# Performance work log

Hardware: AMD Instinct MI355X
Metric: run time of the kernel (lower is better)

The kernel has to match this reference:

```python
import jax, jax.numpy as jnp
import numpy as np

VOCAB = 32000
DIM = 256
LAYERS = 2
CLASSES = 8
BATCH = 32
SEQ = 8192


def setup_inputs() -> dict:
    key = jax.random.key(0)
    ks = jax.random.split(key, 8)
    s = 1.0 / np.sqrt(DIM)
    x = jax.random.randint(ks[0], (BATCH, SEQ), 0, VOCAB, dtype=jnp.int32)
    emb = jax.random.normal(ks[1], (VOCAB, DIM), dtype=jnp.float32)
    Wz = jax.random.normal(ks[2], (LAYERS, DIM, DIM), dtype=jnp.float32) * s
    bz = jnp.zeros((LAYERS, DIM), dtype=jnp.float32)
    Wh = jax.random.normal(ks[3], (LAYERS, DIM, DIM), dtype=jnp.float32) * s
    bh = jnp.zeros((LAYERS, DIM), dtype=jnp.float32)
    Wo = jax.random.normal(ks[4], (DIM, CLASSES), dtype=jnp.float32) * s
    bo = jnp.zeros((CLASSES,), dtype=jnp.float32)
    return {"x": x, "emb": emb, "Wz": Wz, "bz": bz, "Wh": Wh, "bh": bh, "Wo": Wo, "bo": bo}


def _min_gru_layer(h_in, Wz_l, bz_l, Wh_l, bh_l):
    # minGRU: z_t = sigmoid(W_z x_t); h~_t = W_h x_t
    # h_t = (1 - z_t) * h_{t-1} + z_t * h~_t,  h_0 = 0
    z = jax.nn.sigmoid(jnp.einsum('bsd,de->bse', h_in, Wz_l) + bz_l)
    h_tilde = jnp.einsum('bsd,de->bse', h_in, Wh_l) + bh_l
    a = 1.0 - z          # decay coefficient
    b = z * h_tilde      # input contribution
    # parallel associative scan of h_t = a_t * h_{t-1} + b_t (h_0 = 0)
    def combine(c1, c2):
        a1, b1 = c1
        a2, b2 = c2
        return a1 * a2, b1 * a2 + b2
    _, h = jax.lax.associative_scan(combine, (a, b), axis=1)
    return h


def reference(x, emb, Wz, bz, Wh, bh, Wo, bo):
    h = emb[x]  # [B, S, D]
    for l in range(LAYERS):
        h = _min_gru_layer(h, Wz[l], bz[l], Wh[l], bh[l])
    # classifier on the last timestep
    return h[:, -1] @ Wo + bo  # [B, CLASSES]
```

## Files before the change

kernel.cpp:

```cpp
#include <hip/hip_runtime.h>
#include <stdint.h>

#define SEQ 8192
#define CS 64
#define NCH 128
#define NBLK 4096

typedef float f32x4 __attribute__((ext_vector_type(4)));
typedef short short8 __attribute__((ext_vector_type(8)));
typedef unsigned short u16;
typedef u16 ushort8 __attribute__((ext_vector_type(8)));
typedef u16 ushort4v __attribute__((ext_vector_type(4)));

__device__ __forceinline__ u16 f2bf(float f) {
  uint32_t u = __float_as_uint(f);
  u += 0x7fffu + ((u >> 16) & 1u);
  return (u16)(u >> 16);
}

__device__ __forceinline__ void gld16(void* lds, const void* g) {
  __builtin_amdgcn_global_load_lds(
      (const __attribute__((address_space(1))) uint32_t*)g,
      (__attribute__((address_space(3))) uint32_t*)lds, 16, 0, 0);
}

__global__ void embq_kernel(const float* __restrict__ emb, u16* __restrict__ embq) {
  int i = (blockIdx.x * 256 + threadIdx.x) * 4;
  float4 v = *(const float4*)(emb + i);
  ushort4v p;
  p[0] = f2bf(v.x); p[1] = f2bf(v.y); p[2] = f2bf(v.z); p[3] = f2bf(v.w);
  *(ushort4v*)(embq + i) = p;
}

__global__ void wt_kernel(const float* __restrict__ Wz, const float* __restrict__ Wh,
                          u16* __restrict__ WtS) {
  int idx = blockIdx.x * 256 + threadIdx.x;
  int d = idx & 255;
  int k = (idx >> 8) & 255;
  int m = idx >> 16;
  const float* src = (m < 2 ? Wz : Wh) + (size_t)(m & 1) * 65536;
  float v = src[k * 256 + d];
  int dh = d >> 6, dloc = d & 63, k32 = k >> 5, kl = k & 31;
  size_t tile = ((size_t)(m * 4 + dh) * 8 + k32) * 4096;
  size_t byte = (size_t)(dloc * 64 + ((kl * 2) ^ (((dloc >> 1) & 3) << 4)));
  *(u16*)((char*)WtS + tile + byte) = f2bf(v);
}

__device__ __forceinline__ void stage32(char* dst_wave, const char* WtSb, int mat, int k32,
                                        int w, int lane) {
  const char* src = WtSb + ((size_t)((mat * 4 + w) * 8 + k32)) * 4096 + lane * 16;
  #pragma unroll
  for (int i = 0; i < 4; i++)
    gld16(dst_wave + i * 1024, src + i * 1024);
}

__device__ __forceinline__ void load_fa(const u16* As, int k32, int l15, int lg,
                                        short8 (&fa)[4]) {
  const int xm = (l15 & 7) << 4;
  const int kt = k32 >> 1, ks = k32 & 1;
  #pragma unroll
  for (int mi = 0; mi < 4; mi++)
    fa[mi] = *(const short8*)((const char*)As + kt * 8192 +
               (((mi * 16 + l15) * 128 + ks * 64 + lg * 16) ^ xm));
}

__device__ __forceinline__ void mfma_frags(const char* Pw, const short8 (&fa)[4],
    int l15, int lg, f32x4 (&acc)[4][4])
{
  #pragma unroll
  for (int ni = 0; ni < 4; ni++) {
    const int dloc = ni * 16 + l15;
    const int off = dloc * 64 + ((lg * 16) ^ (((dloc >> 1) & 3) << 4));
    short8 fb = *(const short8*)(Pw + off);
    #pragma unroll
    for (int mi = 0; mi < 4; mi++)
      acc[mi][ni] = __builtin_amdgcn_mfma_f32_16x16x32_bf16(fa[mi], fb, acc[mi][ni], 0, 0, 0);
  }
}

__device__ __forceinline__ void gemm_pipe3(int lsel, const char* WtSb, const u16* As,
    char* Pw, int w, int l15, int lg, int lane,
    f32x4 (&accz)[4][4], f32x4 (&acch)[4][4])
{
  stage32(Pw,         WtSb, lsel,     0, w, lane);
  stage32(Pw + 16384, WtSb, 2 + lsel, 0, w, lane);
  short8 fa[4];
  #pragma unroll
  for (int i = 0; i < 16; ++i) {
    if (i < 15) asm volatile("s_waitcnt vmcnt(4)" ::: "memory");
    else        asm volatile("s_waitcnt vmcnt(0)" ::: "memory");
    __builtin_amdgcn_sched_barrier(0);
    if (i + 2 < 16)
      stage32(Pw + ((i + 2) % 3) * 16384, WtSb,
              ((i + 2) & 1) ? (2 + lsel) : lsel, (i + 2) >> 1, w, lane);
    if ((i & 1) == 0) {
      load_fa(As, i >> 1, l15, lg, fa);
      mfma_frags(Pw + (i % 3) * 16384, fa, l15, lg, accz);
    } else {
      mfma_frags(Pw + (i % 3) * 16384, fa, l15, lg, acch);
    }
  }
}

__device__ __forceinline__ float2* seg_ptr(char* segt, int s, int d) {
  return (float2*)(segt + s * 2048 + ((d * 8) ^ (s << 4)));
}

template<int PHASE>
__global__ __launch_bounds__(256, 2)
void gru_kernel(const int* __restrict__ x, const u16* __restrict__ embq,
                const u16* __restrict__ WtS,
                const float* __restrict__ bz0, const float* __restrict__ bh0,
                const float* __restrict__ bz1, const float* __restrict__ bh1,
                const float* __restrict__ carry,
                float* __restrict__ Ap, float* __restrict__ Bs)
{
  __shared__ __align__(16) u16 As[16384];
  __shared__ __align__(16) char Pb[49152];

  const int tid = threadIdx.x;
  const int lane = tid & 63;
  const int w = tid >> 6;
  const int l15 = lane & 15, lg = lane >> 4;
  const int cb = blockIdx.x;
  const int b = cb >> 7, c = cb & (NCH - 1);
  const char* WtSb = (const char*)WtS;
  char* segt = (char*)As;
  char* Pw = Pb + w * 4096;

  {
    const int sm = tid >> 2, kq = tid & 3;
    const int tok = x[b * SEQ + c * CS + sm];
    const u16* src = embq + (size_t)tok * 256 + kq * 64;
    char* sub = (char*)As + kq * 8192;
    const int swz = (sm & 7) << 4;
    #pragma unroll
    for (int j = 0; j < 8; j++) {
      ushort8 p = *(const ushort8*)(src + j * 8);
      *(ushort8*)(sub + ((sm * 128 + j * 16) ^ swz)) = p;
    }
  }

  f32x4 accz[4][4], acch[4][4];
  #pragma unroll
  for (int i = 0; i < 4; i++)
    #pragma unroll
    for (int j = 0; j < 4; j++) {
      f32x4 zz = {0.f, 0.f, 0.f, 0.f};
      accz[i][j] = zz; acch[i][j] = zz;
    }

  __syncthreads();
  gemm_pipe3(0, WtSb, As, Pw, w, l15, lg, lane, accz, acch);
  __syncthreads();

  #pragma unroll
  for (int ni = 0; ni < 4; ni++) {
    const int d = w * 64 + ni * 16 + l15;
    const float bzv = bz0[d];
    const float bhv = bh0[d];
    #pragma unroll
    for (int mi = 0; mi < 4; mi++) {
      float A = 1.f, B = 0.f;
      #pragma unroll
      for (int r = 0; r < 4; r++) {
        float zl = accz[mi][ni][r] + bzv;
        float a = __builtin_amdgcn_rcpf(1.f + __expf(zl));
        float ht = acch[mi][ni][r] + bhv;
        float bb = (1.f - a) * ht;
        if (PHASE == 1) { accz[mi][ni][r] = a; acch[mi][ni][r] = bb; }
        B = B * a + bb;
        A *= a;
      }
      *seg_ptr(segt, mi * 4 + lg, d) = make_float2(A, B);
    }
  }
  __syncthreads();

  if (PHASE == 0) {
    float PA = 1.f, PB = 0.f;
    #pragma unroll
    for (int s = 0; s < 16; s++) {
      float2 v = *seg_ptr(segt, s, tid);
      PB = v.x * PB + v.y;
      PA *= v.x;
    }
    Ap[(size_t)cb * 256 + tid] = PA;
    Bs[(size_t)cb * 256 + tid] = PB;
    return;
  }

  {
    float PA = 1.f, PB = 0.f;
    #pragma unroll
    for (int s = 0; s < 16; s++) {
      float2* p = seg_ptr(segt, s, tid);
      float2 v = *p;
      *p = make_float2(PA, PB);
      PB = v.x * PB + v.y;
      PA *= v.x;
    }
  }
  __syncthreads();

  float ea[4][4], eb[4][4], h0v[4];
  #pragma unroll
  for (int ni = 0; ni < 4; ni++) {
    const int d = w * 64 + ni * 16 + l15;
    h0v[ni] = carry[(size_t)cb * 256 + d];
    #pragma unroll
    for (int mi = 0; mi < 4; mi++) {
      float2 e = *seg_ptr(segt, mi * 4 + lg, d);
      ea[mi][ni] = e.x; eb[mi][ni] = e.y;
    }
  }
  __syncthreads();

  #pragma unroll
  for (int ni = 0; ni < 4; ni++) {
    const int d = w * 64 + ni * 16 + l15;
    char* sub = (char*)As + (d >> 6) * 8192;
    const int kl2 = (d & 63) * 2;
    #pragma unroll
    for (int mi = 0; mi < 4; mi++) {
      float h = ea[mi][ni] * h0v[ni] + eb[mi][ni];
      #pragma unroll
      for (int r = 0; r < 4; r++) {
        h = accz[mi][ni][r] * h + acch[mi][ni][r];
        const int t = mi * 16 + lg * 4 + r;
        *(u16*)(sub + ((t * 128 + kl2) ^ ((t & 7) << 4))) = f2bf(h);
      }
    }
  }

  #pragma unroll
  for (int i = 0; i < 4; i++)
    #pragma unroll
    for (int j = 0; j < 4; j++) {
      f32x4 zz = {0.f, 0.f, 0.f, 0.f};
      accz[i][j] = zz; acch[i][j] = zz;
    }

  __syncthreads();
  gemm_pipe3(1, WtSb, As, Pw, w, l15, lg, lane, accz, acch);
  __syncthreads();

  #pragma unroll
  for (int ni = 0; ni < 4; ni++) {
    const int d = w * 64 + ni * 16 + l15;
    const float bzv = bz1[d];
    const float bhv = bh1[d];
    #pragma unroll
    for (int mi = 0; mi < 4; mi++) {
      float A = 1.f, B = 0.f;
      #pragma unroll
      for (int r = 0; r < 4; r++) {
        float zl = accz[mi][ni][r] + bzv;
        float a = __builtin_amdgcn_rcpf(1.f + __expf(zl));
        float ht = acch[mi][ni][r] + bhv;
        float bb = (1.f - a) * ht;
        B = B * a + bb;
        A *= a;
      }
      *seg_ptr(segt, mi * 4 + lg, d) = make_float2(A, B);
    }
  }
  __syncthreads();
  {
    float PA = 1.f, PB = 0.f;
    #pragma unroll
    for (int s = 0; s < 16; s++) {
      float2 v = *seg_ptr(segt, s, tid);
      PB = v.x * PB + v.y;
      PA *= v.x;
    }
    Ap[(size_t)cb * 256 + tid] = PA;
    Bs[(size_t)cb * 256 + tid] = PB;
  }
}

__global__ void scan2_l0(const float* __restrict__ Ap0, const float* __restrict__ Bs0,
                         float* __restrict__ carry) {
  const int g = blockIdx.x * 256 + threadIdx.x;
  const int b = g >> 8, d = g & 255;
  float h = 0.f;
  for (int c = 0; c < NCH; c++) {
    const size_t idx = (size_t)(b * NCH + c) * 256 + d;
    carry[idx] = h;
    h = Bs0[idx] + Ap0[idx] * h;
  }
}

__global__ void scan2_l1(const float* __restrict__ Ap1, const float* __restrict__ Bs1,
                         float* __restrict__ hlast) {
  const int g = blockIdx.x * 256 + threadIdx.x;
  const int b = g >> 8, d = g & 255;
  float h = 0.f;
  for (int c = 0; c < NCH; c++) {
    const size_t idx = (size_t)(b * NCH + c) * 256 + d;
    h = Bs1[idx] + Ap1[idx] * h;
  }
  hlast[b * 256 + d] = h;
}

__global__ void cls_kernel(const float* __restrict__ hlast, const float* __restrict__ Wo,
                           const float* __restrict__ bo, float* __restrict__ out) {
  const int t = threadIdx.x;
  const int b = t >> 3, c = t & 7;
  float acc = bo[c];
  for (int d = 0; d < 256; d++) acc += hlast[b * 256 + d] * Wo[d * 8 + c];
  out[t] = acc;
}

extern "C" void kernel_launch(void* const* d_in, const int* in_sizes, int n_in,
                              void* d_out, int out_size, void* d_ws, size_t ws_size,
                              hipStream_t stream) {
  (void)in_sizes; (void)n_in; (void)out_size; (void)ws_size;
  const int*   x   = (const int*)d_in[0];
  const float* emb = (const float*)d_in[1];
  const float* Wz  = (const float*)d_in[2];
  const float* bz  = (const float*)d_in[3];
  const float* Wh  = (const float*)d_in[4];
  const float* bh  = (const float*)d_in[5];
  const float* Wo  = (const float*)d_in[6];
  const float* bo  = (const float*)d_in[7];
  float* out = (float*)d_out;
  char* ws = (char*)d_ws;

  u16*   embq  = (u16*)  (ws);
  u16*   WtS   = (u16*)  (ws + 16777216ull);
  float* Ap0   = (float*)(ws + 17301504ull);
  float* Bs0   = (float*)(ws + 21495808ull);
  float* carry = (float*)(ws + 25690112ull);
  float* Ap1   = (float*)(ws + 29884416ull);
  float* Bs1   = (float*)(ws + 34078720ull);
  float* hlast = (float*)(ws + 38273024ull);

  embq_kernel<<<8000, 256, 0, stream>>>(emb, embq);
  wt_kernel<<<1024, 256, 0, stream>>>(Wz, Wh, WtS);

  gru_kernel<0><<<NBLK, 256, 0, stream>>>(
      x, embq, WtS, bz, bh, bz + 256, bh + 256, nullptr, Ap0, Bs0);
  scan2_l0<<<32, 256, 0, stream>>>(Ap0, Bs0, carry);
  gru_kernel<1><<<NBLK, 256, 0, stream>>>(
      x, embq, WtS, bz, bh, bz + 256, bh + 256, carry, Ap1, Bs1);

  scan2_l1<<<32, 256, 0, stream>>>(Ap1, Bs1, hlast);
  cls_kernel<<<1, 256, 0, stream>>>(hlast, Wo, bo, out);
}
```

Baseline: 291.7 us.

## Stash layer-0 gate coefficients in global memory instead of recomputing the layer-0 GEMM

Phase 0 now writes per-timestep (a, b) coefficients as packed bf16 pairs into a workspace buffer. Phase 1 reads them back and runs a simple sequential per-channel recurrence instead of redoing the embedding gather and layer-0 GEMM. To keep that buffer small enough to stay cache-resident, the batch is processed in two halves with separate launches. The trade is extra global traffic, bf16 rounding of the coefficients, and twice as many kernel launches, in exchange for dropping the duplicate layer-0 GEMM.

```diff
diff --git a/kernel.cpp b/kernel.cpp
--- a/kernel.cpp
+++ b/kernel.cpp
@@ -4,7 +4,8 @@
 #define SEQ 8192
 #define CS 64
 #define NCH 128
-#define NBLK 4096
+#define HB2 16
+#define HBLK (HB2 * NCH)
 
 typedef float f32x4 __attribute__((ext_vector_type(4)));
 typedef short short8 __attribute__((ext_vector_type(8)));
@@ -16,6 +17,9 @@
   uint32_t u = __float_as_uint(f);
   u += 0x7fffu + ((u >> 16) & 1u);
   return (u16)(u >> 16);
+}
+__device__ __forceinline__ float bf2f(uint32_t lo16) {
+  return __uint_as_float(lo16 << 16);
 }
 
 __device__ __forceinline__ void gld16(void* lds, const void* g) {
@@ -112,7 +116,7 @@
                 const u16* __restrict__ WtS,
                 const float* __restrict__ bz0, const float* __restrict__ bh0,
                 const float* __restrict__ bz1, const float* __restrict__ bh1,
-                const float* __restrict__ carry,
+                const float* __restrict__ carry, uint32_t* __restrict__ ab,
                 float* __restrict__ Ap, float* __restrict__ Bs)
 {
   __shared__ __align__(16) u16 As[16384];
@@ -128,19 +132,6 @@
   char* segt = (char*)As;
   char* Pw = Pb + w * 4096;
 
-  {
-    const int sm = tid >> 2, kq = tid & 3;
-    const int tok = x[b * SEQ + c * CS + sm];
-    const u16* src = embq + (size_t)tok * 256 + kq * 64;
-    char* sub = (char*)As + kq * 8192;
-    const int swz = (sm & 7) << 4;
-    #pragma unroll
-    for (int j = 0; j < 8; j++) {
-      ushort8 p = *(const ushort8*)(src + j * 8);
-      *(ushort8*)(sub + ((sm * 128 + j * 16) ^ swz)) = p;
-    }
-  }
-
   f32x4 accz[4][4], acch[4][4];
   #pragma unroll
   for (int i = 0; i < 4; i++)
@@ -150,97 +141,74 @@
       accz[i][j] = zz; acch[i][j] = zz;
     }
 
-  __syncthreads();
-  gemm_pipe3(0, WtSb, As, Pw, w, l15, lg, lane, accz, acch);
-  __syncthreads();
-
-  #pragma unroll
-  for (int ni = 0; ni < 4; ni++) {
-    const int d = w * 64 + ni * 16 + l15;
-    const float bzv = bz0[d];
-    const float bhv = bh0[d];
-    #pragma unroll
-    for (int mi = 0; mi < 4; mi++) {
-      float A = 1.f, B = 0.f;
+  if (PHASE == 0) {
+    {
+      const int sm = tid >> 2, kq = tid & 3;
+      const int tok = x[b * SEQ + c * CS + sm];
+      const u16* src = embq + (size_t)tok * 256 + kq * 64;
+      char* sub = (char*)As + kq * 8192;
+      const int swz = (sm & 7) << 4;
       #pragma unroll
-      for (int r = 0; r < 4; r++) {
-        float zl = accz[mi][ni][r] + bzv;
-        float a = __builtin_amdgcn_rcpf(1.f + __expf(zl));
-        float ht = acch[mi][ni][r] + bhv;
-        float bb = (1.f - a) * ht;
-        if (PHASE == 1) { accz[mi][ni][r] = a; acch[mi][ni][r] = bb; }
-        B = B * a + bb;
-        A *= a;
+      for (int j = 0; j < 8; j++) {
+        ushort8 p = *(const ushort8*)(src + j * 8);
+        *(ushort8*)(sub + ((sm * 128 + j * 16) ^ swz)) = p;
       }
-      *seg_ptr(segt, mi * 4 + lg, d) = make_float2(A, B);
-    }
-  }
-  __syncthreads();
-
-  if (PHASE == 0) {
-    float PA = 1.f, PB = 0.f;
-    #pragma unroll
-    for (int s = 0; s < 16; s++) {
-      float2 v = *seg_ptr(segt, s, tid);
-      PB = v.x * PB + v.y;
-      PA *= v.x;
-    }
-    Ap[(size_t)cb * 256 + tid] = PA;
-    Bs[(size_t)cb * 256 + tid] = PB;
+    }
+    __syncthreads();
+    gemm_pipe3(0, WtSb, As, Pw, w, l15, lg, lane, accz, acch);
+    __syncthreads();
+
+    #pragma unroll
+    for (int ni = 0; ni < 4; ni++) {
+      const int d = w * 64 + ni * 16 + l15;
+      const float bzv = bz0[d];
+      const float bhv = bh0[d];
+      #pragma unroll
+      for (int mi = 0; mi < 4; mi++) {
+        float A = 1.f, B = 0.f;
+        #pragma unroll
+        for (int r = 0; r < 4; r++) {
+          float zl = accz[mi][ni][r] + bzv;
+          float a = __builtin_amdgcn_rcpf(1.f + __expf(zl));
+          float ht = acch[mi][ni][r] + bhv;
+          float bb = (1.f - a) * ht;
+          const int t = mi * 16 + lg * 4 + r;
+          ab[(size_t)cb * 16384 + t * 256 + d] =
+              (uint32_t)f2bf(a) | ((uint32_t)f2bf(bb) << 16);
+          B = B * a + bb;
+          A *= a;
+        }
+        *seg_ptr(segt, mi * 4 + lg, d) = make_float2(A, B);
+      }
+    }
+    __syncthreads();
+    {
+      float PA = 1.f, PB = 0.f;
+      #pragma unroll
+      for (int s = 0; s < 16; s++) {
+        float2 v = *seg_ptr(segt, s, tid);
+        PB = v.x * PB + v.y;
+        PA *= v.x;
+      }
+      Ap[(size_t)cb * 256 + tid] = PA;
+      Bs[(size_t)cb * 256 + tid] = PB;
+    }
     return;
   }
 
   {
-    float PA = 1.f, PB = 0.f;
-    #pragma unroll
-    for (int s = 0; s < 16; s++) {
-      float2* p = seg_ptr(segt, s, tid);
-      float2 v = *p;
-      *p = make_float2(PA, PB);
-      PB = v.x * PB + v.y;
-      PA *= v.x;
-    }
-  }
-  __syncthreads();
-
-  float ea[4][4], eb[4][4], h0v[4];
-  #pragma unroll
-  for (int ni = 0; ni < 4; ni++) {
-    const int d = w * 64 + ni * 16 + l15;
-    h0v[ni] = carry[(size_t)cb * 256 + d];
-    #pragma unroll
-    for (int mi = 0; mi < 4; mi++) {
-      float2 e = *seg_ptr(segt, mi * 4 + lg, d);
-      ea[mi][ni] = e.x; eb[mi][ni] = e.y;
-    }
-  }
-  __syncthreads();
-
-  #pragma unroll
-  for (int ni = 0; ni < 4; ni++) {
-    const int d = w * 64 + ni * 16 + l15;
+    const int d = tid;
+    float h = carry[(size_t)cb * 256 + d];
+    const uint32_t* pab = ab + (size_t)cb * 16384 + d;
     char* sub = (char*)As + (d >> 6) * 8192;
     const int kl2 = (d & 63) * 2;
-    #pragma unroll
-    for (int mi = 0; mi < 4; mi++) {
-      float h = ea[mi][ni] * h0v[ni] + eb[mi][ni];
-      #pragma unroll
-      for (int r = 0; r < 4; r++) {
-        h = accz[mi][ni][r] * h + acch[mi][ni][r];
-        const int t = mi * 16 + lg * 4 + r;
-        *(u16*)(sub + ((t * 128 + kl2) ^ ((t & 7) << 4))) = f2bf(h);
-      }
-    }
-  }
-
-  #pragma unroll
-  for (int i = 0; i < 4; i++)
-    #pragma unroll
-    for (int j = 0; j < 4; j++) {
-      f32x4 zz = {0.f, 0.f, 0.f, 0.f};
-      accz[i][j] = zz; acch[i][j] = zz;
-    }
-
+    #pragma unroll 8
+    for (int t = 0; t < CS; t++) {
+      uint32_t u = pab[(size_t)t * 256];
+      h = bf2f(u & 0xffffu) * h + bf2f(u >> 16);
+      *(u16*)(sub + ((t * 128 + kl2) ^ ((t & 7) << 4))) = f2bf(h);
+    }
+  }
   __syncthreads();
   gemm_pipe3(1, WtSb, As, Pw, w, l15, lg, lane, accz, acch);
   __syncthreads();
@@ -327,23 +295,28 @@
   float* out = (float*)d_out;
   char* ws = (char*)d_ws;
 
-  u16*   embq  = (u16*)  (ws);
-  u16*   WtS   = (u16*)  (ws + 16777216ull);
-  float* Ap0   = (float*)(ws + 17301504ull);
-  float* Bs0   = (float*)(ws + 21495808ull);
-  float* carry = (float*)(ws + 25690112ull);
-  float* Ap1   = (float*)(ws + 29884416ull);
-  float* Bs1   = (float*)(ws + 34078720ull);
-  float* hlast = (float*)(ws + 38273024ull);
+  u16*      embq  = (u16*)     (ws);
+  u16*      WtS   = (u16*)     (ws + 16777216ull);
+  float*    Ap0   = (float*)   (ws + 17301504ull);
+  float*    Bs0   = (float*)   (ws + 19398656ull);
+  float*    carry = (float*)   (ws + 21495808ull);
+  float*    Ap1   = (float*)   (ws + 23592960ull);
+  float*    Bs1   = (float*)   (ws + 27787264ull);
+  float*    hlast = (float*)   (ws + 31981568ull);
+  uint32_t* ab    = (uint32_t*)(ws + 32014336ull);
 
   embq_kernel<<<8000, 256, 0, stream>>>(emb, embq);
   wt_kernel<<<1024, 256, 0, stream>>>(Wz, Wh, WtS);
 
-  gru_kernel<0><<<NBLK, 256, 0, stream>>>(
-      x, embq, WtS, bz, bh, bz + 256, bh + 256, nullptr, Ap0, Bs0);
-  scan2_l0<<<32, 256, 0, stream>>>(Ap0, Bs0, carry);
-  gru_kernel<1><<<NBLK, 256, 0, stream>>>(
-      x, embq, WtS, bz, bh, bz + 256, bh + 256, carry, Ap1, Bs1);
+  for (int hf = 0; hf < 2; hf++) {
+    const int* xh = x + (size_t)hf * HB2 * SEQ;
+    gru_kernel<0><<<HBLK, 256, 0, stream>>>(
+        xh, embq, WtS, bz, bh, bz + 256, bh + 256, nullptr, ab, Ap0, Bs0);
+    scan2_l0<<<HB2, 256, 0, stream>>>(Ap0, Bs0, carry);
+    gru_kernel<1><<<HBLK, 256, 0, stream>>>(
+        xh, embq, WtS, bz, bh, bz + 256, bh + 256, carry, ab,
+        Ap1 + (size_t)hf * HBLK * 256, Bs1 + (size_t)hf * HBLK * 256);
+  }
 
   scan2_l1<<<32, 256, 0, stream>>>(Ap1, Bs1, hlast);
   cls_kernel<<<1, 256, 0, stream>>>(hlast, Wo, bo, out);
```

Result: faster. 271.3 us (-7.0%).
